# Kernel optimization log

Hardware: AMD Instinct MI355X
Metric: run time of the kernel (lower is better)

Reference implementation:

```python
import jax, jax.numpy as jnp
import numpy as np

N = 131072
F_IN = 256
FEATURES = 64
N_SOURCES = 32


def setup_inputs() -> dict:
    key = jax.random.key(0)
    k1, k2, k3 = jax.random.split(key, 3)
    x = jax.random.normal(k1, (N, F_IN), dtype=jnp.float32)
    source = jax.random.randint(k2, (N,), 0, N_SOURCES, dtype=jnp.int32)
    W = jax.random.normal(k3, (F_IN, N_SOURCES * FEATURES), dtype=jnp.float32) * (1.0 / np.sqrt(F_IN))
    b = jnp.zeros((N_SOURCES * FEATURES,), dtype=jnp.float32)
    return {"x": x, "source": source, "W": W, "b": b}


def reference(x, source, W, b):
    # Dense projection to all sources: (N, n_sources*features)
    y = jnp.dot(x, W) + b
    # Per-row gather of the slice belonging to this row's source id.
    # Equivalent to y[i, source[i]*FEATURES : (source[i]+1)*FEATURES].
    y = y.reshape(x.shape[0], N_SOURCES, FEATURES)
    out = jnp.take_along_axis(y, source[:, None, None].astype(jnp.int32), axis=1)
    return out[:, 0, :]  # (N, FEATURES)
```

## Files before the change

kernel.cpp:

```cpp
#include <hip/hip_runtime.h>

#define N_ROWS   131072
#define F_IN     256
#define FEAT     64
#define NSRC     32
#define WSTRIDE  (NSRC * FEAT)
#define NCH      32
#define CHUNK    4096
#define LCAP     320
#define NBUCK    (NCH * NSRC)
#define KPAD     264

#define MCHUNK   4096
#define LCAP1    512

typedef __attribute__((ext_vector_type(8))) short  bf16x8;
typedef __attribute__((ext_vector_type(4))) float  f32x4;

__device__ __forceinline__ unsigned short f2bf(float f) {
    union { float f; unsigned u; } c; c.f = f;
    unsigned r = c.u + 0x7fffu + ((c.u >> 16) & 1u);
    return (unsigned short)(r >> 16);
}

__device__ __forceinline__ bf16x8 pack8(f32x4 f0, f32x4 f1) {
    bf16x8 a;
    a[0] = (short)f2bf(f0[0]); a[1] = (short)f2bf(f0[1]);
    a[2] = (short)f2bf(f0[2]); a[3] = (short)f2bf(f0[3]);
    a[4] = (short)f2bf(f1[0]); a[5] = (short)f2bf(f1[1]);
    a[6] = (short)f2bf(f1[2]); a[7] = (short)f2bf(f1[3]);
    return a;
}

__global__ void zero_counts(int* __restrict__ ws) {
    const int i = blockIdx.x * 256 + threadIdx.x;
    if (i < NBUCK) ws[i] = 0;
}

__global__ __launch_bounds__(256)
void compact_kernel(const int* __restrict__ src, int* __restrict__ ws) {
    __shared__ int lcnt[NSRC];
    __shared__ int gbase[NSRC];
    const int tid = threadIdx.x;
    if (tid < NSRC) lcnt[tid] = 0;
    __syncthreads();
    const int row = blockIdx.x * 256 + tid;
    const int s   = src[row];
    const int c   = blockIdx.x >> 4;
    const int p   = atomicAdd(&lcnt[s], 1);
    __syncthreads();
    if (tid < NSRC && lcnt[tid] > 0)
        gbase[tid] = atomicAdd(&ws[c * NSRC + tid], lcnt[tid]);
    __syncthreads();
    const int pos = gbase[s] + p;
    if (pos < LCAP)
        ws[NBUCK + ((size_t)(c * NSRC + s)) * LCAP + pos] = row;
}

__device__ __forceinline__ void gather16(const float* __restrict__ x,
                                         const int* lst, int count, int tile,
                                         int col, int quad, f32x4 av[16]) {
    const int arow = lst[min(tile * 16 + col, count - 1)];
    const float* rp = x + (size_t)arow * F_IN + quad * 8;
    #pragma unroll
    for (int kk = 0; kk < 8; ++kk) {
        av[2 * kk]     = *(const f32x4*)(rp + kk * 32);
        av[2 * kk + 1] = *(const f32x4*)(rp + kk * 32 + 4);
    }
}

__device__ __forceinline__ void compute_store16(
    const f32x4 av[16], const unsigned short* __restrict__ Wt,
    const int* lst, const float bias[4], float* __restrict__ out,
    int tile, int count, int col, int quad) {
    f32x4 acc[4];
    #pragma unroll
    for (int nt = 0; nt < 4; ++nt) acc[nt] = (f32x4){0.f, 0.f, 0.f, 0.f};
    #pragma unroll
    for (int kk = 0; kk < 8; ++kk) {
        const bf16x8 a = pack8(av[2 * kk], av[2 * kk + 1]);
        #pragma unroll
        for (int nt = 0; nt < 4; ++nt) {
            const bf16x8 bb = *(const bf16x8*)&Wt[(nt * 16 + col) * KPAD + kk * 32 + quad * 8];
            acc[nt] = __builtin_amdgcn_mfma_f32_16x16x32_bf16(a, bb, acc[nt], 0, 0, 0);
        }
    }
    #pragma unroll
    for (int reg = 0; reg < 4; ++reg) {
        const int gm = tile * 16 + quad * 4 + reg;
        if (gm < count) {
            const int grow = lst[gm];
            float* op = out + (size_t)grow * FEAT + col;
            #pragma unroll
            for (int nt = 0; nt < 4; ++nt)
                op[nt * 16] = acc[nt][reg] + bias[nt];
        }
    }
}

__global__ __launch_bounds__(256, 2)
void gemm_kernel(const float* __restrict__ x, const float* __restrict__ W,
                 const float* __restrict__ b, const int* __restrict__ ws,
                 float* __restrict__ out) {
    __shared__ __align__(16) unsigned short Wt[FEAT * KPAD];
    __shared__ int lst[LCAP];

    const int tid    = threadIdx.x;
    const int s      = blockIdx.x;
    const int c      = blockIdx.y;
    const int bucket = c * NSRC + s;
    const int count  = min(ws[bucket], LCAP);
    if (count == 0) return;

    const int* gl = ws + NBUCK + (size_t)bucket * LCAP;
    for (int i = tid; i < count; i += 256) lst[i] = gl[i];

    {
        const int n  = tid & 63;
        const int kp = (tid >> 6) * 2;
        #pragma unroll
        for (int k0 = 0; k0 < F_IN; k0 += 8) {
            const int k = k0 + kp;
            const float w0 = W[(size_t)k       * WSTRIDE + s * FEAT + n];
            const float w1 = W[(size_t)(k + 1) * WSTRIDE + s * FEAT + n];
            *(unsigned*)&Wt[n * KPAD + k] = (unsigned)f2bf(w0) | ((unsigned)f2bf(w1) << 16);
        }
    }

    __syncthreads();

    const int lane = tid & 63, w = tid >> 6;
    const int col  = lane & 15, quad = lane >> 4;

    float bias[4];
    #pragma unroll
    for (int nt = 0; nt < 4; ++nt) bias[nt] = b[s * FEAT + nt * 16 + col];

    const int ntiles = (count + 15) >> 4;
    if (w >= ntiles) return;

    f32x4 avA[16], avB[16];
    gather16(x, lst, count, w, col, quad, avA);
    for (int t = w; ; ) {
        const int t1 = t + 4;
        if (t1 < ntiles) gather16(x, lst, count, t1, col, quad, avB);
        compute_store16(avA, Wt, lst, bias, out, t, count, col, quad);
        if (t1 >= ntiles) break;
        const int t2 = t + 8;
        if (t2 < ntiles) gather16(x, lst, count, t2, col, quad, avA);
        compute_store16(avB, Wt, lst, bias, out, t1, count, col, quad);
        if (t2 >= ntiles) break;
        t = t2;
    }
}

__global__ __launch_bounds__(256, 4)
void mono_kernel(const float* __restrict__ x, const int* __restrict__ src,
                 const float* __restrict__ W, const float* __restrict__ b,
                 float* __restrict__ out) {
    __shared__ __align__(16) unsigned short Wt[FEAT * KPAD];
    __shared__ int lst[LCAP1];
    __shared__ int cnt;
    const int tid = threadIdx.x, s = blockIdx.y, chunk0 = blockIdx.x * MCHUNK;
    if (tid == 0) cnt = 0;
    __syncthreads();
    {
        const int n = tid & 63, kp = (tid >> 6) * 2;
        #pragma unroll
        for (int k0 = 0; k0 < F_IN; k0 += 8) {
            const int k = k0 + kp;
            const float w0 = W[(size_t)k * WSTRIDE + s * FEAT + n];
            const float w1 = W[(size_t)(k + 1) * WSTRIDE + s * FEAT + n];
            *(unsigned*)&Wt[n * KPAD + k] = (unsigned)f2bf(w0) | ((unsigned)f2bf(w1) << 16);
        }
    }
    #pragma unroll
    for (int r = 0; r < MCHUNK / 256; ++r) {
        const int row = chunk0 + r * 256 + tid;
        if (src[row] == s) {
            const int p = atomicAdd(&cnt, 1);
            if (p < LCAP1) lst[p] = row;
        }
    }
    __syncthreads();
    const int count = cnt;
    if (count == 0) return;
    const int lane = tid & 63, w = tid >> 6, col = lane & 15, quad = lane >> 4;
    float bias[4];
    #pragma unroll
    for (int nt = 0; nt < 4; ++nt) bias[nt] = b[s * FEAT + nt * 16 + col];
    const int npass = (count + 63) >> 6;
    for (int pp = 0; pp < npass; ++pp) {
        const int base = pp * 64 + w * 16;
        const int ia = lst[min(base + col, count - 1)];
        const float* ap = x + (size_t)ia * F_IN + quad * 8;
        f32x4 av[16];
        #pragma unroll
        for (int kk = 0; kk < 8; ++kk) {
            av[2 * kk]     = *(const f32x4*)(ap + kk * 32);
            av[2 * kk + 1] = *(const f32x4*)(ap + kk * 32 + 4);
        }
        f32x4 acc[4];
        #pragma unroll
        for (int nt = 0; nt < 4; ++nt) acc[nt] = (f32x4){0.f, 0.f, 0.f, 0.f};
        #pragma unroll
        for (int kk = 0; kk < 8; ++kk) {
            const bf16x8 a = pack8(av[2 * kk], av[2 * kk + 1]);
            #pragma unroll
            for (int nt = 0; nt < 4; ++nt) {
                const bf16x8 bb = *(const bf16x8*)&Wt[(nt * 16 + col) * KPAD + kk * 32 + quad * 8];
                acc[nt] = __builtin_amdgcn_mfma_f32_16x16x32_bf16(a, bb, acc[nt], 0, 0, 0);
            }
        }
        #pragma unroll
        for (int reg = 0; reg < 4; ++reg) {
            const int gm = base + quad * 4 + reg;
            if (gm < count) {
                const int row = lst[gm];
                float* op = out + (size_t)row * FEAT;
                #pragma unroll
                for (int nt = 0; nt < 4; ++nt)
                    op[nt * 16 + col] = acc[nt][reg] + bias[nt];
            }
        }
    }
}

extern "C" void kernel_launch(void* const* d_in, const int* in_sizes, int n_in,
                              void* d_out, int out_size, void* d_ws, size_t ws_size,
                              hipStream_t stream) {
    const float* x   = (const float*)d_in[0];
    const int*   src = (const int*)d_in[1];
    const float* W   = (const float*)d_in[2];
    const float* b   = (const float*)d_in[3];
    float*       out = (float*)d_out;

    const size_t ws_needed = (size_t)NBUCK * (1 + LCAP) * sizeof(int);
    if (ws_size >= ws_needed) {
        int* ws = (int*)d_ws;
        zero_counts<<<dim3(4), dim3(256), 0, stream>>>(ws);
        compact_kernel<<<dim3(N_ROWS / 256), dim3(256), 0, stream>>>(src, ws);
        gemm_kernel<<<dim3(NSRC, NCH), dim3(256), 0, stream>>>(x, W, b, ws, out);
    } else {
        mono_kernel<<<dim3(N_ROWS / MCHUNK, NSRC), dim3(256), 0, stream>>>(x, src, W, b, out);
    }
}
```

Baseline: 235.7 us.

## Stage gathered x rows into LDS via async loads, keep W in registers

The bucketed GEMM kernel is restructured. Each block now stages 16 gathered x rows at a time into a double-buffered, XOR-swizzled LDS tile using global_load_lds. Each wave keeps its own 16-column slice of W, converted to bf16, in registers instead of building a transposed bf16 copy of W in LDS. Packed hardware bf16 conversion replaces the software rounding, and launch bounds allow 4 blocks per CU. The aim is to share row gathers across waves and raise occupancy, at the cost of a barrier per 16-row tile and less in-flight memory per wave.

After: 220.4 us. 6.5% less time.

```diff
diff --git a/kernel.cpp b/kernel.cpp
--- a/kernel.cpp
+++ b/kernel.cpp
@@ -9,10 +9,11 @@
 #define CHUNK    4096
 #define LCAP     320
 #define NBUCK    (NCH * NSRC)
-#define KPAD     264
+#define TR       16
 
 #define MCHUNK   4096
 #define LCAP1    512
+#define KPAD     264
 
 typedef __attribute__((ext_vector_type(8))) short  bf16x8;
 typedef __attribute__((ext_vector_type(4))) float  f32x4;
@@ -57,52 +58,56 @@
         ws[NBUCK + ((size_t)(c * NSRC + s)) * LCAP + pos] = row;
 }
 
-__device__ __forceinline__ void gather16(const float* __restrict__ x,
-                                         const int* lst, int count, int tile,
-                                         int col, int quad, f32x4 av[16]) {
-    const int arow = lst[min(tile * 16 + col, count - 1)];
-    const float* rp = x + (size_t)arow * F_IN + quad * 8;
+__device__ __forceinline__ void stage_tile(const float* __restrict__ x,
+                                           const int* lst, int count, int tile,
+                                           int w, int lane, float* Abuf) {
+    #pragma unroll
+    for (int i = 0; i < 4; ++i) {
+        const int r  = w * 4 + i;
+        const int gi = min(tile * TR + r, count - 1);
+        const float* src = x + (size_t)lst[gi] * F_IN + ((lane ^ (r & 7)) << 2);
+        __builtin_amdgcn_global_load_lds(
+            (const __attribute__((address_space(1))) void*)src,
+            (__attribute__((address_space(3))) void*)(Abuf + r * F_IN),
+            16, 0, 0);
+    }
+}
+
+__device__ __forceinline__ void compute_tile(const float* Abuf, const bf16x8 bb[8],
+                                             const int* lst, float bias,
+                                             float* __restrict__ out,
+                                             int tile, int count,
+                                             int w, int col, int quad) {
+    f32x4 acc = (f32x4){0.f, 0.f, 0.f, 0.f};
+    const int key = col & 7;
+    const float* arow = Abuf + col * F_IN;
     #pragma unroll
     for (int kk = 0; kk < 8; ++kk) {
-        av[2 * kk]     = *(const f32x4*)(rp + kk * 32);
-        av[2 * kk + 1] = *(const f32x4*)(rp + kk * 32 + 4);
-    }
-}
-
-__device__ __forceinline__ void compute_store16(
-    const f32x4 av[16], const unsigned short* __restrict__ Wt,
-    const int* lst, const float bias[4], float* __restrict__ out,
-    int tile, int count, int col, int quad) {
-    f32x4 acc[4];
-    #pragma unroll
-    for (int nt = 0; nt < 4; ++nt) acc[nt] = (f32x4){0.f, 0.f, 0.f, 0.f};
-    #pragma unroll
-    for (int kk = 0; kk < 8; ++kk) {
-        const bf16x8 a = pack8(av[2 * kk], av[2 * kk + 1]);
-        #pragma unroll
-        for (int nt = 0; nt < 4; ++nt) {
-            const bf16x8 bb = *(const bf16x8*)&Wt[(nt * 16 + col) * KPAD + kk * 32 + quad * 8];
-            acc[nt] = __builtin_amdgcn_mfma_f32_16x16x32_bf16(a, bb, acc[nt], 0, 0, 0);
-        }
+        const int s0 = kk * 8 + quad * 2;
+        const f32x4 lo = *(const f32x4*)(arow + (((s0    ) ^ key) << 2));
+        const f32x4 hi = *(const f32x4*)(arow + (((s0 + 1) ^ key) << 2));
+        unsigned u0, u1, u2, u3;
+        asm("v_cvt_pk_bf16_f32 %0, %1, %2" : "=v"(u0) : "v"(lo[0]), "v"(lo[1]));
+        asm("v_cvt_pk_bf16_f32 %0, %1, %2" : "=v"(u1) : "v"(lo[2]), "v"(lo[3]));
+        asm("v_cvt_pk_bf16_f32 %0, %1, %2" : "=v"(u2) : "v"(hi[0]), "v"(hi[1]));
+        asm("v_cvt_pk_bf16_f32 %0, %1, %2" : "=v"(u3) : "v"(hi[2]), "v"(hi[3]));
+        union { unsigned u[4]; bf16x8 v; } cv;
+        cv.u[0] = u0; cv.u[1] = u1; cv.u[2] = u2; cv.u[3] = u3;
+        acc = __builtin_amdgcn_mfma_f32_16x16x32_bf16(cv.v, bb[kk], acc, 0, 0, 0);
     }
     #pragma unroll
     for (int reg = 0; reg < 4; ++reg) {
-        const int gm = tile * 16 + quad * 4 + reg;
-        if (gm < count) {
-            const int grow = lst[gm];
-            float* op = out + (size_t)grow * FEAT + col;
-            #pragma unroll
-            for (int nt = 0; nt < 4; ++nt)
-                op[nt * 16] = acc[nt][reg] + bias[nt];
-        }
-    }
-}
-
-__global__ __launch_bounds__(256, 2)
+        const int gm = tile * TR + quad * 4 + reg;
+        if (gm < count)
+            out[(size_t)lst[gm] * FEAT + w * 16 + col] = acc[reg] + bias;
+    }
+}
+
+__global__ __launch_bounds__(256, 4)
 void gemm_kernel(const float* __restrict__ x, const float* __restrict__ W,
                  const float* __restrict__ b, const int* __restrict__ ws,
                  float* __restrict__ out) {
-    __shared__ __align__(16) unsigned short Wt[FEAT * KPAD];
+    __shared__ __align__(16) float A[2][TR][F_IN];
     __shared__ int lst[LCAP];
 
     const int tid    = threadIdx.x;
@@ -115,42 +120,41 @@
     const int* gl = ws + NBUCK + (size_t)bucket * LCAP;
     for (int i = tid; i < count; i += 256) lst[i] = gl[i];
 
-    {
-        const int n  = tid & 63;
-        const int kp = (tid >> 6) * 2;
-        #pragma unroll
-        for (int k0 = 0; k0 < F_IN; k0 += 8) {
-            const int k = k0 + kp;
-            const float w0 = W[(size_t)k       * WSTRIDE + s * FEAT + n];
-            const float w1 = W[(size_t)(k + 1) * WSTRIDE + s * FEAT + n];
-            *(unsigned*)&Wt[n * KPAD + k] = (unsigned)f2bf(w0) | ((unsigned)f2bf(w1) << 16);
-        }
-    }
-
-    __syncthreads();
-
     const int lane = tid & 63, w = tid >> 6;
     const int col  = lane & 15, quad = lane >> 4;
 
-    float bias[4];
-    #pragma unroll
-    for (int nt = 0; nt < 4; ++nt) bias[nt] = b[s * FEAT + nt * 16 + col];
-
-    const int ntiles = (count + 15) >> 4;
-    if (w >= ntiles) return;
-
-    f32x4 avA[16], avB[16];
-    gather16(x, lst, count, w, col, quad, avA);
-    for (int t = w; ; ) {
-        const int t1 = t + 4;
-        if (t1 < ntiles) gather16(x, lst, count, t1, col, quad, avB);
-        compute_store16(avA, Wt, lst, bias, out, t, count, col, quad);
-        if (t1 >= ntiles) break;
-        const int t2 = t + 8;
-        if (t2 < ntiles) gather16(x, lst, count, t2, col, quad, avA);
-        compute_store16(avB, Wt, lst, bias, out, t1, count, col, quad);
-        if (t2 >= ntiles) break;
-        t = t2;
+    __syncthreads();
+
+    const int ntiles = (count + TR - 1) / TR;
+
+    stage_tile(x, lst, count, 0, w, lane, &A[0][0][0]);
+
+    bf16x8 bb[8];
+    {
+        const float* wp = W + (size_t)(quad * 8) * WSTRIDE + s * FEAT + w * 16 + col;
+        #pragma unroll
+        for (int kk = 0; kk < 8; ++kk) {
+            float t[8];
+            #pragma unroll
+            for (int j = 0; j < 8; ++j)
+                t[j] = wp[(size_t)(kk * 32 + j) * WSTRIDE];
+            bf16x8 v;
+            #pragma unroll
+            for (int j = 0; j < 8; ++j) v[j] = (short)f2bf(t[j]);
+            bb[kk] = v;
+        }
+    }
+    const float bias = b[s * FEAT + w * 16 + col];
+
+    __syncthreads();
+
+    int buf = 0;
+    for (int t = 0; t < ntiles; ++t) {
+        if (t + 1 < ntiles)
+            stage_tile(x, lst, count, t + 1, w, lane, &A[buf ^ 1][0][0]);
+        compute_tile(&A[buf][0][0], bb, lst, bias, out, t, count, w, col, quad);
+        __syncthreads();
+        buf ^= 1;
     }
 }
 
```
